# Optimization experiments

Measured on AMD Instinct MI355X. Metric: run time of the kernel, lower is better.

## Reference

```python
import jax, jax.numpy as jnp
import numpy as np


def setup_inputs() -> dict:
    key = jax.random.key(0)
    k1, k2, k3 = jax.random.split(key, 3)
    B, D, F, P = 4096, 1024, 2048, 1024
    return {
        "x": jax.random.normal(k1, (B, D), dtype=jnp.float32),
        "features": jax.random.normal(k2, (F, D), dtype=jnp.float32),
        "prototypes": jax.random.normal(k3, (P, D), dtype=jnp.float32),
        "alpha": jnp.ones((1,), dtype=jnp.float32),
        "beta": jnp.ones((1,), dtype=jnp.float32),
        "theta": jnp.ones((1,), dtype=jnp.float32),
    }


def reference(x, features, prototypes, alpha, beta, theta):
    # Project each set ONCE (the original redundantly broadcasts first).
    xf = x @ features.T            # [B, F]
    pf = prototypes @ features.T   # [P, F]
    sx = jax.nn.sigmoid(xf)        # x_present [B, F]
    sp = jax.nn.sigmoid(pf)        # p_present [P, F]
    ax = xf * sx                   # [B, F]
    bp = pf * sp                   # [P, F]
    # common[b,p]        = sum_f xf*pf*sx*sp            = (xf*sx) @ (pf*sp)^T
    # x_distinct[b,p]    = sum_f xf*sx*(1-sp)           = rowsum(xf*sx) - (xf*sx) @ sp^T
    # p_distinct[b,p]    = sum_f pf*sp*(1-sx)           = rowsum(pf*sp) - sx @ (pf*sp)^T
    common = ax @ bp.T                                     # [B, P]
    x_distinctive = ax.sum(axis=1, keepdims=True) - ax @ sp.T  # [B, P]
    p_distinctive = bp.sum(axis=1)[None, :] - sx @ bp.T        # [B, P]
    return theta * common - alpha * x_distinctive - beta * p_distinctive
```

## Files before the change

### kernel.cpp

```cpp
#include <hip/hip_runtime.h>
#include <hip/hip_bf16.h>

typedef __bf16 bf16_t;
typedef bf16_t bf16x4 __attribute__((ext_vector_type(4)));
typedef bf16_t bf16x8 __attribute__((ext_vector_type(8)));
typedef float f32x4 __attribute__((ext_vector_type(4)));

#define AS1 __attribute__((address_space(1)))
#define AS3 __attribute__((address_space(3)))

__device__ __forceinline__ void gload_lds16(const void* g, void* l) {
    __builtin_amdgcn_global_load_lds((const AS1 void*)g, (AS3 void*)l, 16, 0, 0);
}
__device__ __forceinline__ void gload_lds4(const void* g, void* l) {
    __builtin_amdgcn_global_load_lds((const AS1 void*)g, (AS3 void*)l, 4, 0, 0);
}

__device__ __forceinline__ float sigmoidf_(float v) {
    return 1.0f / (1.0f + __expf(-v));
}

__global__ __launch_bounds__(256) void k_convert3(const float* __restrict__ x,
                                                  const float* __restrict__ pr,
                                                  const float* __restrict__ ft,
                                                  bf16_t* __restrict__ dst) {
    const int n4 = 7168 * 256;
    int i = blockIdx.x * 256 + threadIdx.x;
    const int stride = gridDim.x * 256;
    for (; i < n4; i += stride) {
        float4 v;
        if (i < 1048576) v = ((const float4*)x)[i];
        else if (i < 1310720) v = ((const float4*)pr)[i - 1048576];
        else v = ((const float4*)ft)[i - 1310720];
        bf16x4 o;
        o[0] = (bf16_t)v.x; o[1] = (bf16_t)v.y; o[2] = (bf16_t)v.z; o[3] = (bf16_t)v.w;
        ((bf16x4*)dst)[i] = o;
    }
}

__global__ __launch_bounds__(256) void k_foldrs(const float* __restrict__ rsPart,
                                                float* __restrict__ rsums) {
    const int r = blockIdx.x * 256 + threadIdx.x;
    float s = 0.f;
#pragma unroll
    for (int b = 0; b < 8; ++b) s += rsPart[b * 5120 + r];
    rsums[r] = s;
}

__global__ __launch_bounds__(256) void k_reduce4(const bf16_t* __restrict__ part,
                                                 const float* __restrict__ rsums,
                                                 const float* __restrict__ pa,
                                                 float* __restrict__ out) {
    const int idx = blockIdx.x * 256 + threadIdx.x;
    const int region = idx >> 13;
    const int widx = idx & 8191;
    const int wv = widx >> 10;
    const int chunk = (widx >> 6) & 15;
    const int ln = widx & 63;
    const int bx = region >> 2, by = region & 3;
    const int wm = wv >> 2, wn = wv & 3;
    const int fg = chunk >> 1, gp = chunk & 1;
    const int er = (ln >> 4) << 2, ec = ln & 15;
    const long off = (long)idx * 8;

    float sum[8] = {};
#pragma unroll
    for (int s = 0; s < 4; ++s) {
        bf16x8 v = *(const bf16x8*)(part + (long)s * 4194304 + off);
#pragma unroll
        for (int j = 0; j < 8; ++j) sum[j] += (float)v[j];
    }
    const int r0 = bx * 256 + wm * 128 + fg * 16 + er;
    const int c0 = by * 256 + wn * 64 + gp * 32 + ec;
    const float a = pa[0];
#pragma unroll
    for (int q = 0; q < 4; ++q) {
        const float ra = a * rsums[r0 + q];
#pragma unroll
        for (int gh = 0; gh < 2; ++gh) {
            const int c = c0 + gh * 16;
            out[(long)(r0 + q) * 1024 + c] = sum[gh * 4 + q] - ra - rsums[4096 + c];
        }
    }
}

constexpr int SLICE = 16384;

__global__ __launch_bounds__(512, 2) void gemm2_8p(
    const bf16_t* __restrict__ A, const bf16_t* __restrict__ B,
    int NT, long ldab, long ldbb, bf16_t* __restrict__ O1, long zstride) {
    __shared__ char lds[131072];
    const int tid = threadIdx.x;
    const int wave = tid >> 6, lane = tid & 63;
    const int wm = wave >> 2, wn = wave & 3;

    const int gx = gridDim.x, gy = gridDim.y;
    const int o = blockIdx.x + gx * (blockIdx.y + gy * blockIdx.z);
    const int cpx = (gx * gy * (int)gridDim.z) >> 3;
    const int v = (o & 7) * cpx + (o >> 3);
    const int bx = v % gx;
    const int rem = v / gx;
    const int by = rem % gy;
    const int bz = rem / gy;

    const long bm = (long)bx * 256, bn = (long)by * 256;
    const int kb0 = bz * NT * 64;
    const char* Ab = (const char*)A + bm * ldab;
    const char* Bb = (const char*)B + bn * ldbb;

    const int swzcb = ((lane >> 4) << 4) ^ (((lane >> 3) & 1) << 5);
    const int base_a = (wm * 128 + (lane & 15)) * 64 + swzcb;
    const int base_b = (wn * 64 + (lane & 15)) * 64 + swzcb;

    f32x4 acc[8][4] = {};

    auto STAGE = [&](const char* gb, long ld, int kbyte, int ldsoff) {
#pragma unroll
        for (int j = 0; j < 2; ++j) {
            const int oo = (j * 512 + tid) << 4;
            const int r = oo >> 6;
            const int cb = (oo & 63) ^ (((oo >> 9) & 1) << 5);
            gload_lds16(gb + (long)r * ld + kbyte + cb, lds + ldsoff + (oo & ~1023));
        }
    };

#define KB(t, s) ((kb0 + (t) * 64 + (s) * 32) * 2)
#define LOFF(b, ab, s) ((((b) * 2 + (ab)) * 2 + (s)) * SLICE)
#define VM4 asm volatile("s_waitcnt vmcnt(4)" ::: "memory")
#define VM0 asm volatile("s_waitcnt vmcnt(0)" ::: "memory")

    auto PF = [&](int t1, int s, int nb) {
        STAGE(Ab, ldab, KB(t1, s), LOFF(nb, 0, s));
        STAGE(Bb, ldbb, KB(t1, s), LOFF(nb, 1, s));
    };

#define PHASE2(Sl, PFSTMT, WAITSTMT)                                            \
    do {                                                                        \
        const int sA = LOFF(cur, 0, Sl);                                        \
        const int sB = LOFF(cur, 1, Sl);                                        \
        bf16x8 af[8];                                                           \
        bf16x8 bfr[4];                                                          \
        _Pragma("unroll") for (int f = 0; f < 8; ++f)                           \
            af[f] = *(const bf16x8*)(lds + sA + base_a + f * 1024);             \
        _Pragma("unroll") for (int g = 0; g < 4; ++g)                           \
            bfr[g] = *(const bf16x8*)(lds + sB + base_b + g * 1024);            \
        PFSTMT;                                                                 \
        __builtin_amdgcn_sched_barrier(0);                                      \
        __builtin_amdgcn_s_barrier();                                           \
        __builtin_amdgcn_s_setprio(1);                                          \
        _Pragma("unroll") for (int f = 0; f < 8; ++f)                           \
            _Pragma("unroll") for (int g = 0; g < 4; ++g)                       \
                acc[f][g] = __builtin_amdgcn_mfma_f32_16x16x32_bf16(            \
                    af[f], bfr[g], acc[f][g], 0, 0, 0);                         \
        __builtin_amdgcn_s_setprio(0);                                          \
        __builtin_amdgcn_sched_barrier(0);                                      \
        WAITSTMT;                                                               \
        __builtin_amdgcn_s_barrier();                                           \
    } while (0)

    int cur = 0;
    STAGE(Ab, ldab, KB(0, 0), LOFF(0, 0, 0));
    STAGE(Bb, ldbb, KB(0, 0), LOFF(0, 1, 0));
    STAGE(Ab, ldab, KB(0, 1), LOFF(0, 0, 1));
    STAGE(Bb, ldbb, KB(0, 1), LOFF(0, 1, 1));
    VM4;
    __builtin_amdgcn_s_barrier();

    for (int t = 0; t < NT - 1; ++t) {
        const int nb = cur ^ 1;
        PHASE2(0, PF(t + 1, 0, nb), VM4);
        PHASE2(1, PF(t + 1, 1, nb), VM4);
        cur = nb;
    }
    PHASE2(0, , VM0);
    PHASE2(1, , );

#undef PHASE2
#undef KB
#undef LOFF

    bf16_t* Op = O1 + (long)bz * zstride + (long)(bx * 4 + by) * 65536 +
                 wave * 8192 + lane * 8;
#pragma unroll
    for (int fg = 0; fg < 8; ++fg)
#pragma unroll
        for (int gp = 0; gp < 2; ++gp) {
            bf16x8 w;
#pragma unroll
            for (int gh = 0; gh < 2; ++gh)
#pragma unroll
                for (int q = 0; q < 4; ++q)
                    w[gh * 4 + q] = (bf16_t)acc[fg][gp * 2 + gh][q];
            *(bf16x8*)(Op + (fg * 2 + gp) * 512) = w;
        }
#undef VM4
#undef VM0
}

__global__ __launch_bounds__(512, 2) void gemm1_160(
    const bf16_t* __restrict__ A, const bf16_t* __restrict__ B,
    bf16_t* __restrict__ O1, bf16_t* __restrict__ O1b,
    float* __restrict__ rsPart,
    const float* __restrict__ pa, const float* __restrict__ pb,
    const float* __restrict__ pt) {
    __shared__ char lds[106496];
    const int tid = threadIdx.x;
    const int wave = tid >> 6, lane = tid & 63;
    const int wm = wave >> 2, wn = wave & 3;
    const int NT = 16;

    const int gx = gridDim.x, gy = gridDim.y;
    const int o = blockIdx.x + gx * blockIdx.y;
    const int cpx = (gx * gy) >> 3;
    const int v = (o & 7) * cpx + (o >> 3);
    const int bx = v % gx;
    const int by = v / gx;

    const long bm = (long)bx * 160, bn = (long)by * 256;
    const char* Ab = (const char*)A + bm * 2048;
    const char* Bb = (const char*)B + bn * 2048;

    const int swzcb = ((lane >> 4) << 4) ^ (((lane >> 3) & 1) << 5);
    const int base_a = (wm * 80 + (lane & 15)) * 64 + swzcb;
    const int base_b = (wn * 64 + (lane & 15)) * 64 + swzcb;

    f32x4 acc[5][4] = {};

    auto STAGE_A = [&](int kbyte, int ldsoff) {
        {
            const int oo = tid << 4;
            const int r = oo >> 6;
            const int cb = (oo & 63) ^ (((oo >> 9) & 1) << 5);
            gload_lds16(Ab + (long)r * 2048 + kbyte + cb, lds + ldsoff + (oo & ~1023));
        }
        {
            const int oo = 8192 + (tid << 2);
            const int r = oo >> 6;
            const int cb = (oo & 63) ^ (((oo >> 9) & 1) << 5);
            gload_lds4(Ab + (long)r * 2048 + kbyte + cb, lds + ldsoff + 8192 + wave * 256);
        }
    };
    auto STAGE_B = [&](int kbyte, int ldsoff) {
#pragma unroll
        for (int j = 0; j < 2; ++j) {
            const int oo = (j * 512 + tid) << 4;
            const int r = oo >> 6;
            const int cb = (oo & 63) ^ (((oo >> 9) & 1) << 5);
            gload_lds16(Bb + (long)r * 2048 + kbyte + cb, lds + ldsoff + (oo & ~1023));
        }
    };

#define KB1(t, s) (((t) * 64 + (s) * 32) * 2)
#define LOFF_A(b, s) (((b) * 2 + (s)) * 10240)
#define LOFF_B(b, s) (40960 + ((b) * 2 + (s)) * 16384)
#define VM4 asm volatile("s_waitcnt vmcnt(4)" ::: "memory")
#define VM0 asm volatile("s_waitcnt vmcnt(0)" ::: "memory")

    auto PF1 = [&](int t1, int s, int nb) {
        STAGE_A(KB1(t1, s), LOFF_A(nb, s));
        STAGE_B(KB1(t1, s), LOFF_B(nb, s));
    };

#define PHASE1(Sl, PFSTMT, WAITSTMT)                                            \
    do {                                                                        \
        const int sA = LOFF_A(cur, Sl);                                         \
        const int sB = LOFF_B(cur, Sl);                                         \
        bf16x8 af[5];                                                           \
        bf16x8 bfr[4];                                                          \
        _Pragma("unroll") for (int f = 0; f < 5; ++f)                           \
            af[f] = *(const bf16x8*)(lds + sA + base_a + f * 1024);             \
        _Pragma("unroll") for (int g = 0; g < 4; ++g)                           \
            bfr[g] = *(const bf16x8*)(lds + sB + base_b + g * 1024);            \
        PFSTMT;                                                                 \
        __builtin_amdgcn_sched_barrier(0);                                      \
        __builtin_amdgcn_s_barrier();                                           \
        __builtin_amdgcn_s_setprio(1);                                          \
        _Pragma("unroll") for (int f = 0; f < 5; ++f)                           \
            _Pragma("unroll") for (int g = 0; g < 4; ++g)                       \
                acc[f][g] = __builtin_amdgcn_mfma_f32_16x16x32_bf16(            \
                    bfr[g], af[f], acc[f][g], 0, 0, 0);                         \
        __builtin_amdgcn_s_setprio(0);                                          \
        __builtin_amdgcn_sched_barrier(0);                                      \
        WAITSTMT;                                                               \
        __builtin_amdgcn_s_barrier();                                           \
    } while (0)

    int cur = 0;
    STAGE_A(KB1(0, 0), LOFF_A(0, 0));
    STAGE_B(KB1(0, 0), LOFF_B(0, 0));
    STAGE_A(KB1(0, 1), LOFF_A(0, 1));
    STAGE_B(KB1(0, 1), LOFF_B(0, 1));
    VM4;
    __builtin_amdgcn_s_barrier();

    for (int t = 0; t < NT - 1; ++t) {
        const int nb = cur ^ 1;
        PHASE1(0, PF1(t + 1, 0, nb), VM4);
        PHASE1(1, PF1(t + 1, 1, nb), VM4);
        cur = nb;
    }
    PHASE1(0, , VM0);
    PHASE1(1, , );

#undef PHASE1
#undef KB1
#undef LOFF_A
#undef LOFF_B
#undef VM4
#undef VM0

    const float va = pa[0], vb = pb[0], vt = pt[0];
    const int lm = lane & 15;
    const int ln4 = (lane >> 4) << 2;
    char* wlds = lds + 4096 + wave * 4096;
    const int wswz = (lm & 7) << 4;
    float rs[5];
#pragma unroll
    for (int f = 0; f < 5; ++f) rs[f] = 0.f;

#pragma unroll
    for (int mf = 0; mf < 5; ++mf) {
        const long growbase = bm + wm * 80 + mf * 16;
        const bool isXf = (growbase < 4096);
        bf16_t* gb = isXf ? O1 : O1b;
        const long rbase0 = isXf ? growbase : (growbase - 4096);
#pragma unroll
        for (int g = 0; g < 4; ++g) {
            bf16x4 w0, w1;
#pragma unroll
            for (int q = 0; q < 4; ++q) {
                const float vv = acc[mf][g][q];
                const float s = sigmoidf_(vv);
                const float prod = vv * s;
                w0[q] = (bf16_t)(isXf ? prod : (vt * prod + va * s));
                w1[q] = (bf16_t)(isXf ? s : (vb * prod));
                rs[mf] += isXf ? prod : vb * prod;
            }
            const int a = lm * 128 + ((g * 32 + ln4 * 2) ^ wswz);
            *(bf16x4*)(wlds + a) = w0;
            *(bf16x4*)(wlds + 2048 + a) = w1;
        }
#pragma unroll
        for (int rd = 0; rd < 2; ++rd) {
            const int row = rd * 8 + (lane >> 3);
            const int a = row * 128 + (((lane & 7) * 16) ^ ((row & 7) << 4));
            bf16x8 v0 = *(const bf16x8*)(wlds + a);
            bf16x8 v1 = *(const bf16x8*)(wlds + 2048 + a);
            bf16_t* dst = gb + (rbase0 + row) * 4096 + bn + wn * 64 + (lane & 7) * 8;
            *(bf16x8*)dst = v0;
            *(bf16x8*)(dst + 2048) = v1;
        }
    }

    float* lds_f = (float*)lds;
#pragma unroll
    for (int f = 0; f < 5; ++f) {
        float t = rs[f];
        t += __shfl_xor(t, 16);
        t += __shfl_xor(t, 32);
        if ((lane >> 4) == 0) lds_f[wn * 160 + wm * 80 + f * 16 + lm] = t;
    }
    __syncthreads();
    if (tid < 160) {
        const float s = lds_f[tid] + lds_f[160 + tid] + lds_f[320 + tid] + lds_f[480 + tid];
        rsPart[(long)by * 5120 + bm + tid] = s;
    }
}

extern "C" void kernel_launch(void* const* d_in, const int* in_sizes, int n_in,
                              void* d_out, int out_size, void* d_ws, size_t ws_size,
                              hipStream_t stream) {
    const float* x = (const float*)d_in[0];
    const float* feats = (const float*)d_in[1];
    const float* protos = (const float*)d_in[2];
    const float* pa = (const float*)d_in[3];
    const float* pb = (const float*)d_in[4];
    const float* pt = (const float*)d_in[5];
    float* out = (float*)d_out;

    constexpr long Bsz = 4096, D = 1024, F = 2048, P = 1024;

    bf16_t* XP = (bf16_t*)d_ws;
    bf16_t* F16 = XP + (Bsz + P) * D;
    bf16_t* A2 = F16 + F * D;
    bf16_t* B2 = A2 + Bsz * 2 * F;
    float* rsums = (float*)(B2 + P * 2 * F);
    bf16_t* part = (bf16_t*)(rsums + Bsz + P);
    float* rsPart = (float*)(part + 4L * Bsz * P);

    k_convert3<<<2048, 256, 0, stream>>>(x, protos, feats, XP);

    gemm1_160<<<dim3(32, 8), 512, 0, stream>>>(XP, F16, A2, B2, rsPart, pa, pb, pt);

    k_foldrs<<<20, 256, 0, stream>>>(rsPart, rsums);

    gemm2_8p<<<dim3(Bsz / 256, P / 256, 4), 512, 0, stream>>>(
        A2, B2, (int)(2 * F / 64 / 4), 2 * F * 2, 2 * F * 2, part, (long)Bsz * P);

    k_reduce4<<<2048, 256, 0, stream>>>(part, rsums, pa, out);
}
```

Measured before the change: 94.66 us.

## Replace double-buffered K pipeline with 4-slot ring prefetching three slices ahead

Both GEMM kernels move from a two-buffer, two-slice-per-step schedule with two barriers per phase to a 4-slot circular LDS ring. Each phase waits for its data with vmcnt(8) and one barrier, then issues the prefetch for slice p+3. The aim is to keep more global-to-LDS loads in flight and halve the barriers per slice, hiding memory latency behind MFMA work. It relies on correct vmcnt accounting with three slices outstanding. A barrier is added before gemm1's epilogue because that epilogue reuses LDS.

```diff
diff --git a/kernel.cpp b/kernel.cpp
--- a/kernel.cpp
+++ b/kernel.cpp
@@ -84,8 +84,6 @@
     }
 }
 
-constexpr int SLICE = 16384;
-
 __global__ __launch_bounds__(512, 2) void gemm2_8p(
     const bf16_t* __restrict__ A, const bf16_t* __restrict__ B,
     int NT, long ldab, long ldbb, bf16_t* __restrict__ O1, long zstride) {
@@ -124,29 +122,32 @@
         }
     };
 
-#define KB(t, s) ((kb0 + (t) * 64 + (s) * 32) * 2)
-#define LOFF(b, ab, s) ((((b) * 2 + (ab)) * 2 + (s)) * SLICE)
+#define VM8 asm volatile("s_waitcnt vmcnt(8)" ::: "memory")
 #define VM4 asm volatile("s_waitcnt vmcnt(4)" ::: "memory")
 #define VM0 asm volatile("s_waitcnt vmcnt(0)" ::: "memory")
 
-    auto PF = [&](int t1, int s, int nb) {
-        STAGE(Ab, ldab, KB(t1, s), LOFF(nb, 0, s));
-        STAGE(Bb, ldbb, KB(t1, s), LOFF(nb, 1, s));
-    };
-
-#define PHASE2(Sl, PFSTMT, WAITSTMT)                                            \
+    auto PFETCH = [&](int pf) {
+        const int kbyte = (kb0 + pf * 32) * 2;
+        const int ps = pf & 3;
+        STAGE(Ab, ldab, kbyte, ps * 16384);
+        STAGE(Bb, ldbb, kbyte, 65536 + ps * 16384);
+    };
+
+#define PHASE2(p, WAITSTMT, DOPF)                                               \
     do {                                                                        \
-        const int sA = LOFF(cur, 0, Sl);                                        \
-        const int sB = LOFF(cur, 1, Sl);                                        \
+        WAITSTMT;                                                               \
+        __builtin_amdgcn_s_barrier();                                           \
+        const int slot = (p) & 3;                                               \
+        const char* sA = lds + slot * 16384;                                    \
+        const char* sB = lds + 65536 + slot * 16384;                            \
         bf16x8 af[8];                                                           \
         bf16x8 bfr[4];                                                          \
         _Pragma("unroll") for (int f = 0; f < 8; ++f)                           \
-            af[f] = *(const bf16x8*)(lds + sA + base_a + f * 1024);             \
+            af[f] = *(const bf16x8*)(sA + base_a + f * 1024);                   \
         _Pragma("unroll") for (int g = 0; g < 4; ++g)                           \
-            bfr[g] = *(const bf16x8*)(lds + sB + base_b + g * 1024);            \
-        PFSTMT;                                                                 \
+            bfr[g] = *(const bf16x8*)(sB + base_b + g * 1024);                  \
+        if (DOPF) PFETCH((p) + 3);                                              \
         __builtin_amdgcn_sched_barrier(0);                                      \
-        __builtin_amdgcn_s_barrier();                                           \
         __builtin_amdgcn_s_setprio(1);                                          \
         _Pragma("unroll") for (int f = 0; f < 8; ++f)                           \
             _Pragma("unroll") for (int g = 0; g < 4; ++g)                       \
@@ -154,30 +155,22 @@
                     af[f], bfr[g], acc[f][g], 0, 0, 0);                         \
         __builtin_amdgcn_s_setprio(0);                                          \
         __builtin_amdgcn_sched_barrier(0);                                      \
-        WAITSTMT;                                                               \
-        __builtin_amdgcn_s_barrier();                                           \
     } while (0)
 
-    int cur = 0;
-    STAGE(Ab, ldab, KB(0, 0), LOFF(0, 0, 0));
-    STAGE(Bb, ldbb, KB(0, 0), LOFF(0, 1, 0));
-    STAGE(Ab, ldab, KB(0, 1), LOFF(0, 0, 1));
-    STAGE(Bb, ldbb, KB(0, 1), LOFF(0, 1, 1));
-    VM4;
-    __builtin_amdgcn_s_barrier();
-
-    for (int t = 0; t < NT - 1; ++t) {
-        const int nb = cur ^ 1;
-        PHASE2(0, PF(t + 1, 0, nb), VM4);
-        PHASE2(1, PF(t + 1, 1, nb), VM4);
-        cur = nb;
-    }
-    PHASE2(0, , VM0);
-    PHASE2(1, , );
+    const int NP = NT * 2;
+    PFETCH(0);
+    PFETCH(1);
+    PFETCH(2);
+
+    for (int p = 0; p < NP - 3; ++p) PHASE2(p, VM8, 1);
+    PHASE2(NP - 3, VM8, 0);
+    PHASE2(NP - 2, VM4, 0);
+    PHASE2(NP - 1, VM0, 0);
 
 #undef PHASE2
-#undef KB
-#undef LOFF
+#undef VM8
+#undef VM4
+#undef VM0
 
     bf16_t* Op = O1 + (long)bz * zstride + (long)(bx * 4 + by) * 65536 +
                  wave * 8192 + lane * 8;
@@ -193,8 +186,6 @@
                     w[gh * 4 + q] = (bf16_t)acc[fg][gp * 2 + gh][q];
             *(bf16x8*)(Op + (fg * 2 + gp) * 512) = w;
         }
-#undef VM4
-#undef VM0
 }
 
 __global__ __launch_bounds__(512, 2) void gemm1_160(
@@ -250,30 +241,32 @@
         }
     };
 
-#define KB1(t, s) (((t) * 64 + (s) * 32) * 2)
-#define LOFF_A(b, s) (((b) * 2 + (s)) * 10240)
-#define LOFF_B(b, s) (40960 + ((b) * 2 + (s)) * 16384)
+#define VM8 asm volatile("s_waitcnt vmcnt(8)" ::: "memory")
 #define VM4 asm volatile("s_waitcnt vmcnt(4)" ::: "memory")
 #define VM0 asm volatile("s_waitcnt vmcnt(0)" ::: "memory")
 
-    auto PF1 = [&](int t1, int s, int nb) {
-        STAGE_A(KB1(t1, s), LOFF_A(nb, s));
-        STAGE_B(KB1(t1, s), LOFF_B(nb, s));
-    };
-
-#define PHASE1(Sl, PFSTMT, WAITSTMT)                                            \
+    auto PFETCH = [&](int pf) {
+        const int kbyte = pf * 64;
+        const int ps = pf & 3;
+        STAGE_A(kbyte, ps * 10240);
+        STAGE_B(kbyte, 40960 + ps * 16384);
+    };
+
+#define PHASE1(p, WAITSTMT, DOPF)                                               \
     do {                                                                        \
-        const int sA = LOFF_A(cur, Sl);                                         \
-        const int sB = LOFF_B(cur, Sl);                                         \
+        WAITSTMT;                                                               \
+        __builtin_amdgcn_s_barrier();                                           \
+        const int slot = (p) & 3;                                               \
+        const char* sA = lds + slot * 10240;                                    \
+        const char* sB = lds + 40960 + slot * 16384;                            \
         bf16x8 af[5];                                                           \
         bf16x8 bfr[4];                                                          \
         _Pragma("unroll") for (int f = 0; f < 5; ++f)                           \
-            af[f] = *(const bf16x8*)(lds + sA + base_a + f * 1024);             \
+            af[f] = *(const bf16x8*)(sA + base_a + f * 1024);                   \
         _Pragma("unroll") for (int g = 0; g < 4; ++g)                           \
-            bfr[g] = *(const bf16x8*)(lds + sB + base_b + g * 1024);            \
-        PFSTMT;                                                                 \
+            bfr[g] = *(const bf16x8*)(sB + base_b + g * 1024);                  \
+        if (DOPF) PFETCH((p) + 3);                                              \
         __builtin_amdgcn_sched_barrier(0);                                      \
-        __builtin_amdgcn_s_barrier();                                           \
         __builtin_amdgcn_s_setprio(1);                                          \
         _Pragma("unroll") for (int f = 0; f < 5; ++f)                           \
             _Pragma("unroll") for (int g = 0; g < 4; ++g)                       \
@@ -281,33 +274,24 @@
                     bfr[g], af[f], acc[f][g], 0, 0, 0);                         \
         __builtin_amdgcn_s_setprio(0);                                          \
         __builtin_amdgcn_sched_barrier(0);                                      \
-        WAITSTMT;                                                               \
-        __builtin_amdgcn_s_barrier();                                           \
     } while (0)
 
-    int cur = 0;
-    STAGE_A(KB1(0, 0), LOFF_A(0, 0));
-    STAGE_B(KB1(0, 0), LOFF_B(0, 0));
-    STAGE_A(KB1(0, 1), LOFF_A(0, 1));
-    STAGE_B(KB1(0, 1), LOFF_B(0, 1));
-    VM4;
-    __builtin_amdgcn_s_barrier();
-
-    for (int t = 0; t < NT - 1; ++t) {
-        const int nb = cur ^ 1;
-        PHASE1(0, PF1(t + 1, 0, nb), VM4);
-        PHASE1(1, PF1(t + 1, 1, nb), VM4);
-        cur = nb;
-    }
-    PHASE1(0, , VM0);
-    PHASE1(1, , );
+    const int NP = NT * 2;
+    PFETCH(0);
+    PFETCH(1);
+    PFETCH(2);
+
+    for (int p = 0; p < NP - 3; ++p) PHASE1(p, VM8, 1);
+    PHASE1(NP - 3, VM8, 0);
+    PHASE1(NP - 2, VM4, 0);
+    PHASE1(NP - 1, VM0, 0);
 
 #undef PHASE1
-#undef KB1
-#undef LOFF_A
-#undef LOFF_B
+#undef VM8
 #undef VM4
 #undef VM0
+
+    __syncthreads();
 
     const float va = pa[0], vb = pb[0], vt = pt[0];
     const int lm = lane & 15;
```

New measurement: 92.51 us. 2.3% less time.
